# Optimization experiments

Hardware: AMD Instinct MI355X
Metric: run time of the kernel (lower is better)

Reference implementation:

```python
import jax, jax.numpy as jnp
import numpy as np

# ---- static configuration (mirrors init_kwargs) ----
C_IN = 1
SEQ_LEN = 512
N_KERNELS = 10000
KSS = [7, 9, 11]
KS_MAX = max(KSS)
BATCH = 8


def _make_params(seed=42):
    """Replicates the random kernel generation in RocketFeaturesPytorch.__init__."""
    rng = np.random.RandomState(seed)
    ks = np.empty(N_KERNELS, np.int32)
    dil = np.empty(N_KERNELS, np.int32)
    pad = np.empty(N_KERNELS, np.int32)  # per-side padding actually applied (= 2*padding)
    W = np.zeros((N_KERNELS, C_IN, KS_MAX), np.float32)  # zero-padded to KS_MAX taps
    b = np.empty(N_KERNELS, np.float32)
    for i in range(N_KERNELS):
        k = int(rng.choice(KSS))
        d_f = 2.0 ** rng.uniform(0, np.log2((SEQ_LEN - 1) // (k - 1)))
        d = int(d_f)  # Conv1d dilation uses int(dilation)
        p = int((k - 1) * d_f // 2) if rng.randint(2) == 1 else 0  # padding uses FLOAT dilation (as in source)
        w = rng.randn(1, C_IN, k).astype(np.float32)
        w -= w.mean()
        W[i, :, :k] = w[0]
        b[i] = np.float32(2.0 * (rng.rand() - 0.5))
        ks[i], dil[i], pad[i] = k, d, 2 * p  # layer padding = 2*padding per side
    lo = SEQ_LEN + 2 * pad - dil * (ks - 1)  # per-kernel output length (>=1 guaranteed)
    return W, b, ks, dil, pad, lo

_W, _B, _KS, _DIL, _PAD, _LO = _make_params()
PAD_MAX = int(_PAD.max())
T_MAX = int(_LO.max())


def setup_inputs() -> dict:
    key = jax.random.key(0)
    x = jax.random.normal(key, (BATCH, C_IN, SEQ_LEN), dtype=jnp.float32)
    return {
        "x": x,
        "weights": jnp.asarray(_W),                     # [K, C, KS_MAX]
        "biases": jnp.asarray(_B),                      # [K]
        "base": jnp.asarray(PAD_MAX - _PAD, jnp.int32), # [K] start offset into padded x
        "dil": jnp.asarray(_DIL, jnp.int32),            # [K]
        "lo": jnp.asarray(_LO, jnp.int32),              # [K] valid output length
    }


def reference(x, weights, biases, base, dil, lo):
    B, C, L = x.shape
    K = weights.shape[0]
    xpad = jnp.pad(x, ((0, 0), (0, 0), (PAD_MAX, PAD_MAX)))  # [B, C, Lp]
    Lp = xpad.shape[-1]
    t = jnp.arange(T_MAX, dtype=jnp.int32)                   # [T]

    # dilated conv for all kernels at once: out[b,k,t] = sum_{c,j} w[k,c,j] * xpad[b,c, base[k]+t+j*dil[k]]
    acc = jnp.zeros((B, K, T_MAX), x.dtype)
    for j in range(KS_MAX):  # small static loop over taps
        idx = jnp.clip(base[:, None] + t[None, :] + j * dil[:, None], 0, Lp - 1)  # [K, T]
        g = xpad[:, :, idx]                                   # [B, C, K, T]
        acc = acc + jnp.einsum('bckt,kc->bkt', g, weights[:, :, j])
    out = acc + biases[None, :, None]                         # [B, K, T]

    valid = t[None, :] < lo[:, None]                          # [K, T]
    maxs = jnp.max(jnp.where(valid[None], out, -jnp.inf), axis=-1)                       # [B, K]
    ppv = jnp.sum(jnp.where(valid[None], out > 0, False), axis=-1) / lo[None, :].astype(x.dtype)  # [B, K]

    # original interleaves (max_i, ppv_i) per kernel along the feature dim
    return jnp.stack([maxs, ppv.astype(x.dtype)], axis=-1).reshape(B, 2 * K)
```

## Files before the change

kernel.cpp:

```cpp
#include <hip/hip_runtime.h>
#include <math.h>

#define NK     10000
#define NBATCH 8
#define LSEQ   512
#define KSMAX  11
#define RED_STRIDE 20
#define SM_DW  (256 * RED_STRIDE + 256)

typedef _Float16 half2v __attribute__((ext_vector_type(2)));

__global__ __launch_bounds__(1024) void reduce_max_base(const int* __restrict__ base, int n,
                                                        int* __restrict__ outv) {
    __shared__ int red[16];
    int tid = threadIdx.x;
    int m = 0;
    for (int i = tid; i < n; i += 1024) m = max(m, base[i]);
    #pragma unroll
    for (int off = 32; off > 0; off >>= 1) m = max(m, __shfl_down(m, off));
    if ((tid & 63) == 0) red[tid >> 6] = m;
    __syncthreads();
    if (tid == 0) {
        int r = red[0];
        #pragma unroll
        for (int i = 1; i < 16; ++i) r = max(r, red[i]);
        *outv = r;
    }
}

template <int KS>
__device__ __forceinline__ void run_conv(const float4* __restrict__ rows,
                                         const half2v* __restrict__ wh, half2v bb,
                                         int pad, int dl, int lk,
                                         int wave, int lane,
                                         half2v& m0, half2v& m1, half2v& m2, half2v& m3,
                                         half2v& c0, half2v& c1, half2v& c2, half2v& c3) {
    const half2v one2  = {(_Float16)1.0f, (_Float16)1.0f};
    const half2v zero2 = {(_Float16)0.0f, (_Float16)0.0f};
    const half2v big2  = {(_Float16)16384.0f, (_Float16)16384.0f};
    for (int t0 = wave * 64; t0 < lk; t0 += 256) {
        const int t = t0 + lane;
        half2v a0 = bb, a1 = bb, a2 = bb, a3 = bb;
        int pos = t - pad;
        #pragma unroll
        for (int j = 0; j < KS; ++j) {
            int pc = min(max(pos, -1), LSEQ);
            float4 r = rows[pc + 1];
            half2v v0 = ((half2v*)&r)[0];
            half2v v1 = ((half2v*)&r)[1];
            half2v v2 = ((half2v*)&r)[2];
            half2v v3 = ((half2v*)&r)[3];
            half2v wj = wh[j];
            a0 += wj * v0;
            a1 += wj * v1;
            a2 += wj * v2;
            a3 += wj * v3;
            pos += dl;
        }
        if (t < lk) {
            m0 = __builtin_elementwise_max(m0, a0);
            m1 = __builtin_elementwise_max(m1, a1);
            m2 = __builtin_elementwise_max(m2, a2);
            m3 = __builtin_elementwise_max(m3, a3);
            c0 += __builtin_elementwise_min(__builtin_elementwise_max(a0 * big2, zero2), one2);
            c1 += __builtin_elementwise_min(__builtin_elementwise_max(a1 * big2, zero2), one2);
            c2 += __builtin_elementwise_min(__builtin_elementwise_max(a2 * big2, zero2), one2);
            c3 += __builtin_elementwise_min(__builtin_elementwise_max(a3 * big2, zero2), one2);
        }
    }
}

__global__ __launch_bounds__(256) void rocket_kernel(
    const float* __restrict__ x, const float* __restrict__ W,
    const float* __restrict__ bias, const int* __restrict__ base,
    const int* __restrict__ dil, const int* __restrict__ lo,
    const int* __restrict__ padmax_p, float* __restrict__ out) {
    __shared__ __align__(16) float sm[SM_DW];
    const int tid = threadIdx.x;
    const int k = blockIdx.x;

    #pragma unroll
    for (int i = 0; i < 2; ++i) {
        int p = tid + i * 256;
        half2v h0 = {(_Float16)x[0 * LSEQ + p], (_Float16)x[1 * LSEQ + p]};
        half2v h1 = {(_Float16)x[2 * LSEQ + p], (_Float16)x[3 * LSEQ + p]};
        half2v h2 = {(_Float16)x[4 * LSEQ + p], (_Float16)x[5 * LSEQ + p]};
        half2v h3 = {(_Float16)x[6 * LSEQ + p], (_Float16)x[7 * LSEQ + p]};
        float4 v;
        ((half2v*)&v)[0] = h0;
        ((half2v*)&v)[1] = h1;
        ((half2v*)&v)[2] = h2;
        ((half2v*)&v)[3] = h3;
        *(float4*)(sm + (size_t)(p + 1) * 4) = v;
    }
    if (tid < 4)           sm[tid] = 0.0f;
    else if (tid < 8)      sm[513 * 4 + (tid - 4)] = 0.0f;

    float w[KSMAX];
    half2v wh[KSMAX];
    #pragma unroll
    for (int j = 0; j < KSMAX; ++j) {
        w[j] = W[(size_t)k * KSMAX + j];
        _Float16 wf = (_Float16)w[j];
        wh[j] = (half2v){wf, wf};
    }
    _Float16 bf = (_Float16)bias[k];
    const half2v bb = {bf, bf};
    const int dl = dil[k];
    const int lk = lo[k];
    const int pad = *padmax_p - base[k];

    __syncthreads();

    const int wave = tid >> 6;
    const int lane = tid & 63;

    half2v mneg = {(_Float16)(-INFINITY), (_Float16)(-INFINITY)};
    half2v zz   = {(_Float16)0.0f, (_Float16)0.0f};
    half2v m0 = mneg, m1 = mneg, m2 = mneg, m3 = mneg;
    half2v c0 = zz,   c1 = zz,   c2 = zz,   c3 = zz;

    const bool z7 = (w[7] == 0.0f) && (w[8] == 0.0f) && (w[9] == 0.0f) && (w[10] == 0.0f);
    const bool z9 = (w[9] == 0.0f) && (w[10] == 0.0f);
    const float4* rows = (const float4*)sm;
    if (z7)      run_conv<7 >(rows, wh, bb, pad, dl, lk, wave, lane, m0, m1, m2, m3, c0, c1, c2, c3);
    else if (z9) run_conv<9 >(rows, wh, bb, pad, dl, lk, wave, lane, m0, m1, m2, m3, c0, c1, c2, c3);
    else         run_conv<11>(rows, wh, bb, pad, dl, lk, wave, lane, m0, m1, m2, m3, c0, c1, c2, c3);

    __syncthreads();
    {
        float* red = sm;
        int tb = tid * RED_STRIDE;
        float4 fm0 = {(float)m0.x, (float)m0.y, (float)m1.x, (float)m1.y};
        float4 fm1 = {(float)m2.x, (float)m2.y, (float)m3.x, (float)m3.y};
        float4 fc0 = {(float)c0.x, (float)c0.y, (float)c1.x, (float)c1.y};
        float4 fc1 = {(float)c2.x, (float)c2.y, (float)c3.x, (float)c3.y};
        *(float4*)(red + tb + 0)  = fm0;
        *(float4*)(red + tb + 4)  = fm1;
        *(float4*)(red + tb + 8)  = fc0;
        *(float4*)(red + tb + 12) = fc1;
        __syncthreads();
        int v = tid >> 4;
        int sub = tid & 15;
        bool ismax = v < 8;
        float r = ismax ? -INFINITY : 0.0f;
        #pragma unroll
        for (int i = 0; i < 16; ++i) {
            float xv = red[(sub + 16 * i) * RED_STRIDE + v];
            r = ismax ? fmaxf(r, xv) : (r + xv);
        }
        __syncthreads();
        red[256 * RED_STRIDE + v * 16 + sub] = r;
        __syncthreads();
        if (tid < 16) {
            const float4* p = (const float4*)(red + 256 * RED_STRIDE + tid * 16);
            float4 q0 = p[0], q1 = p[1], q2 = p[2], q3 = p[3];
            float r2;
            int b = tid & 7;
            if (tid < 8) {
                r2 = fmaxf(fmaxf(fmaxf(q0.x, q0.y), fmaxf(q0.z, q0.w)),
                           fmaxf(fmaxf(q1.x, q1.y), fmaxf(q1.z, q1.w)));
                r2 = fmaxf(r2, fmaxf(fmaxf(fmaxf(q2.x, q2.y), fmaxf(q2.z, q2.w)),
                                     fmaxf(fmaxf(q3.x, q3.y), fmaxf(q3.z, q3.w))));
                out[(size_t)b * (2 * NK) + 2 * k] = r2;
            } else {
                r2 = (q0.x + q0.y + q0.z + q0.w) + (q1.x + q1.y + q1.z + q1.w)
                   + (q2.x + q2.y + q2.z + q2.w) + (q3.x + q3.y + q3.z + q3.w);
                out[(size_t)b * (2 * NK) + 2 * k + 1] = r2 / (float)lk;
            }
        }
    }
}

extern "C" void kernel_launch(void* const* d_in, const int* in_sizes, int n_in,
                              void* d_out, int out_size, void* d_ws, size_t ws_size,
                              hipStream_t stream) {
    const float* x    = (const float*)d_in[0];
    const float* W    = (const float*)d_in[1];
    const float* bias = (const float*)d_in[2];
    const int*   base = (const int*)d_in[3];
    const int*   dil  = (const int*)d_in[4];
    const int*   lo   = (const int*)d_in[5];
    float* out = (float*)d_out;
    int* padmax = (int*)d_ws;

    reduce_max_base<<<1, 1024, 0, stream>>>(base, in_sizes[3], padmax);
    rocket_kernel<<<NK, 256, 0, stream>>>(x, W, bias, base, dil, lo, padmax, out);
}
```

Measured before the change: 93.33 us.

## Map one ROCKET kernel per wave, derive padding locally, drop max-reduce launch

Each 256-thread block now handles four convolution kernels, one per wave, instead of one kernel per block. The shared fp16 copy of x is staged once and reused by all four. Per-kernel padding is computed from lo, dilation and kernel size, which removes the separate max-reduction launch over base. The cross-block-thread LDS reduction with several barriers becomes a per-wave LDS pass plus xor shuffles in fp16. This cuts launch overhead, staging cost and synchronisation, at the risk of load imbalance between waves whose kernels have different output lengths.

```diff
diff --git a/kernel.cpp b/kernel.cpp
--- a/kernel.cpp
+++ b/kernel.cpp
@@ -1,44 +1,27 @@
 #include <hip/hip_runtime.h>
 #include <math.h>
 
-#define NK     10000
-#define NBATCH 8
-#define LSEQ   512
-#define KSMAX  11
-#define RED_STRIDE 20
-#define SM_DW  (256 * RED_STRIDE + 256)
+#define NK      10000
+#define LSEQ    512
+#define KSMAX   11
+#define ROWS_DW (514 * 4)
+#define RED_OFF ROWS_DW
+#define SM_DW   (ROWS_DW + 256 * 10)
 
 typedef _Float16 half2v __attribute__((ext_vector_type(2)));
 
-__global__ __launch_bounds__(1024) void reduce_max_base(const int* __restrict__ base, int n,
-                                                        int* __restrict__ outv) {
-    __shared__ int red[16];
-    int tid = threadIdx.x;
-    int m = 0;
-    for (int i = tid; i < n; i += 1024) m = max(m, base[i]);
-    #pragma unroll
-    for (int off = 32; off > 0; off >>= 1) m = max(m, __shfl_down(m, off));
-    if ((tid & 63) == 0) red[tid >> 6] = m;
-    __syncthreads();
-    if (tid == 0) {
-        int r = red[0];
-        #pragma unroll
-        for (int i = 1; i < 16; ++i) r = max(r, red[i]);
-        *outv = r;
-    }
-}
+union H2U { half2v h; unsigned int u; };
 
 template <int KS>
 __device__ __forceinline__ void run_conv(const float4* __restrict__ rows,
                                          const half2v* __restrict__ wh, half2v bb,
-                                         int pad, int dl, int lk,
-                                         int wave, int lane,
+                                         int pad, int dl, int lk, int lane,
                                          half2v& m0, half2v& m1, half2v& m2, half2v& m3,
                                          half2v& c0, half2v& c1, half2v& c2, half2v& c3) {
     const half2v one2  = {(_Float16)1.0f, (_Float16)1.0f};
     const half2v zero2 = {(_Float16)0.0f, (_Float16)0.0f};
     const half2v big2  = {(_Float16)16384.0f, (_Float16)16384.0f};
-    for (int t0 = wave * 64; t0 < lk; t0 += 256) {
+    for (int t0 = 0; t0 < lk; t0 += 64) {
         const int t = t0 + lane;
         half2v a0 = bb, a1 = bb, a2 = bb, a3 = bb;
         int pos = t - pad;
@@ -46,15 +29,11 @@
         for (int j = 0; j < KS; ++j) {
             int pc = min(max(pos, -1), LSEQ);
             float4 r = rows[pc + 1];
-            half2v v0 = ((half2v*)&r)[0];
-            half2v v1 = ((half2v*)&r)[1];
-            half2v v2 = ((half2v*)&r)[2];
-            half2v v3 = ((half2v*)&r)[3];
             half2v wj = wh[j];
-            a0 += wj * v0;
-            a1 += wj * v1;
-            a2 += wj * v2;
-            a3 += wj * v3;
+            a0 += wj * ((half2v*)&r)[0];
+            a1 += wj * ((half2v*)&r)[1];
+            a2 += wj * ((half2v*)&r)[2];
+            a3 += wj * ((half2v*)&r)[3];
             pos += dl;
         }
         if (t < lk) {
@@ -72,12 +51,13 @@
 
 __global__ __launch_bounds__(256) void rocket_kernel(
     const float* __restrict__ x, const float* __restrict__ W,
-    const float* __restrict__ bias, const int* __restrict__ base,
-    const int* __restrict__ dil, const int* __restrict__ lo,
-    const int* __restrict__ padmax_p, float* __restrict__ out) {
+    const float* __restrict__ bias, const int* __restrict__ dil,
+    const int* __restrict__ lo, float* __restrict__ out) {
     __shared__ __align__(16) float sm[SM_DW];
-    const int tid = threadIdx.x;
-    const int k = blockIdx.x;
+    const int tid  = threadIdx.x;
+    const int wave = tid >> 6;
+    const int lane = tid & 63;
+    const int k    = blockIdx.x * 4 + wave;
 
     #pragma unroll
     for (int i = 0; i < 2; ++i) {
@@ -108,12 +88,8 @@
     const half2v bb = {bf, bf};
     const int dl = dil[k];
     const int lk = lo[k];
-    const int pad = *padmax_p - base[k];
 
     __syncthreads();
-
-    const int wave = tid >> 6;
-    const int lane = tid & 63;
 
     half2v mneg = {(_Float16)(-INFINITY), (_Float16)(-INFINITY)};
     half2v zz   = {(_Float16)0.0f, (_Float16)0.0f};
@@ -123,50 +99,60 @@
     const bool z7 = (w[7] == 0.0f) && (w[8] == 0.0f) && (w[9] == 0.0f) && (w[10] == 0.0f);
     const bool z9 = (w[9] == 0.0f) && (w[10] == 0.0f);
     const float4* rows = (const float4*)sm;
-    if (z7)      run_conv<7 >(rows, wh, bb, pad, dl, lk, wave, lane, m0, m1, m2, m3, c0, c1, c2, c3);
-    else if (z9) run_conv<9 >(rows, wh, bb, pad, dl, lk, wave, lane, m0, m1, m2, m3, c0, c1, c2, c3);
-    else         run_conv<11>(rows, wh, bb, pad, dl, lk, wave, lane, m0, m1, m2, m3, c0, c1, c2, c3);
+    if (z7) {
+        int pad = (lk - LSEQ + dl * 6) >> 1;
+        run_conv<7 >(rows, wh, bb, pad, dl, lk, lane, m0, m1, m2, m3, c0, c1, c2, c3);
+    } else if (z9) {
+        int pad = (lk - LSEQ + dl * 8) >> 1;
+        run_conv<9 >(rows, wh, bb, pad, dl, lk, lane, m0, m1, m2, m3, c0, c1, c2, c3);
+    } else {
+        int pad = (lk - LSEQ + dl * 10) >> 1;
+        run_conv<11>(rows, wh, bb, pad, dl, lk, lane, m0, m1, m2, m3, c0, c1, c2, c3);
+    }
 
-    __syncthreads();
     {
-        float* red = sm;
-        int tb = tid * RED_STRIDE;
-        float4 fm0 = {(float)m0.x, (float)m0.y, (float)m1.x, (float)m1.y};
-        float4 fm1 = {(float)m2.x, (float)m2.y, (float)m3.x, (float)m3.y};
-        float4 fc0 = {(float)c0.x, (float)c0.y, (float)c1.x, (float)c1.y};
-        float4 fc1 = {(float)c2.x, (float)c2.y, (float)c3.x, (float)c3.y};
-        *(float4*)(red + tb + 0)  = fm0;
-        *(float4*)(red + tb + 4)  = fm1;
-        *(float4*)(red + tb + 8)  = fc0;
-        *(float4*)(red + tb + 12) = fc1;
-        __syncthreads();
-        int v = tid >> 4;
-        int sub = tid & 15;
-        bool ismax = v < 8;
-        float r = ismax ? -INFINITY : 0.0f;
+        unsigned int* red = (unsigned int*)(sm + RED_OFF);
+        const int tb = tid * 10;
+        H2U u0, u1, u2, u3;
+        uint2 p01, p23;
+        u0.h = m0; u1.h = m1; u2.h = m2; u3.h = m3;
+        p01.x = u0.u; p01.y = u1.u; p23.x = u2.u; p23.y = u3.u;
+        *(uint2*)(red + tb + 0) = p01;
+        *(uint2*)(red + tb + 2) = p23;
+        u0.h = c0; u1.h = c1; u2.h = c2; u3.h = c3;
+        p01.x = u0.u; p01.y = u1.u; p23.x = u2.u; p23.y = u3.u;
+        *(uint2*)(red + tb + 4) = p01;
+        *(uint2*)(red + tb + 6) = p23;
+
+        const int q  = lane & 7;
+        const int dv = lane >> 3;
+        const bool ismax = dv < 4;
+        const int wbase = (tid & ~63) * 10;
+        half2v r = ismax ? (half2v){(_Float16)(-INFINITY), (_Float16)(-INFINITY)}
+                         : (half2v){(_Float16)0.0f, (_Float16)0.0f};
         #pragma unroll
-        for (int i = 0; i < 16; ++i) {
-            float xv = red[(sub + 16 * i) * RED_STRIDE + v];
-            r = ismax ? fmaxf(r, xv) : (r + xv);
+        for (int i = 0; i < 8; ++i) {
+            H2U t;
+            t.u = red[wbase + (q + 8 * i) * 10 + dv];
+            r = ismax ? __builtin_elementwise_max(r, t.h) : (r + t.h);
         }
-        __syncthreads();
-        red[256 * RED_STRIDE + v * 16 + sub] = r;
-        __syncthreads();
-        if (tid < 16) {
-            const float4* p = (const float4*)(red + 256 * RED_STRIDE + tid * 16);
-            float4 q0 = p[0], q1 = p[1], q2 = p[2], q3 = p[3];
-            float r2;
-            int b = tid & 7;
-            if (tid < 8) {
-                r2 = fmaxf(fmaxf(fmaxf(q0.x, q0.y), fmaxf(q0.z, q0.w)),
-                           fmaxf(fmaxf(q1.x, q1.y), fmaxf(q1.z, q1.w)));
-                r2 = fmaxf(r2, fmaxf(fmaxf(fmaxf(q2.x, q2.y), fmaxf(q2.z, q2.w)),
-                                     fmaxf(fmaxf(q3.x, q3.y), fmaxf(q3.z, q3.w))));
-                out[(size_t)b * (2 * NK) + 2 * k] = r2;
+        #pragma unroll
+        for (int s = 1; s < 8; s <<= 1) {
+            H2U me, ot;
+            me.h = r;
+            ot.u = (unsigned int)__shfl_xor((int)me.u, s, 64);
+            r = ismax ? __builtin_elementwise_max(r, ot.h) : (r + ot.h);
+        }
+        if (q == 0) {
+            if (ismax) {
+                int b = 2 * dv;
+                out[(size_t)b       * (2 * NK) + 2 * k] = (float)r.x;
+                out[(size_t)(b + 1) * (2 * NK) + 2 * k] = (float)r.y;
             } else {
-                r2 = (q0.x + q0.y + q0.z + q0.w) + (q1.x + q1.y + q1.z + q1.w)
-                   + (q2.x + q2.y + q2.z + q2.w) + (q3.x + q3.y + q3.z + q3.w);
-                out[(size_t)b * (2 * NK) + 2 * k + 1] = r2 / (float)lk;
+                int b = 2 * (dv - 4);
+                float inv = 1.0f / (float)lk;
+                out[(size_t)b       * (2 * NK) + 2 * k + 1] = (float)r.x * inv;
+                out[(size_t)(b + 1) * (2 * NK) + 2 * k + 1] = (float)r.y * inv;
             }
         }
     }
@@ -178,12 +164,9 @@
     const float* x    = (const float*)d_in[0];
     const float* W    = (const float*)d_in[1];
     const float* bias = (const float*)d_in[2];
-    const int*   base = (const int*)d_in[3];
     const int*   dil  = (const int*)d_in[4];
     const int*   lo   = (const int*)d_in[5];
     float* out = (float*)d_out;
-    int* padmax = (int*)d_ws;
 
-    reduce_max_base<<<1, 1024, 0, stream>>>(base, in_sizes[3], padmax);
-    rocket_kernel<<<NK, 256, 0, stream>>>(x, W, bias, base, dil, lo, padmax, out);
+    rocket_kernel<<<NK / 4, 256, 0, stream>>>(x, W, bias, dil, lo, out);
 }
```

New measurement: 84.79 us. 9.1% less time.
